# Kernel optimization log

Measured on AMD Instinct MI355X. Metric: run time of the kernel, lower is better.

Reference implementation:

```python
import jax, jax.numpy as jnp
import numpy as np

B, C, HF, WF = 2, 128, 60, 80
N = 3072
T = 16.0          # min(t_base + epoch, t_max), saturated
WIN_HALF = 0.125  # config['window_size'] (normalized half-width)
WIN_STEPS = 9     # window sampling grid side
EPS = 1e-6

def l2norm(x, axis):
    return x / jnp.sqrt(jnp.sum(x * x, axis=axis, keepdims=True) + 1e-12)

def denorm(cn, h, w):
    # normalized [-1,1] (x,y) -> pixel coords
    return (cn + 1.0) * 0.5 * jnp.array([w - 1.0, h - 1.0], cn.dtype)

def norm_coords(c, h, w):
    return c * (2.0 / jnp.array([w - 1.0, h - 1.0], c.dtype)) - 1.0

def bilinear_sample(fmap, cn):
    """fmap (b,C,H,W); cn (b,M,2) normalized (x,y); align_corners=True, border pad."""
    b, Cc, H, W = fmap.shape
    x = (cn[..., 0] + 1.0) * 0.5 * (W - 1)
    y = (cn[..., 1] + 1.0) * 0.5 * (H - 1)
    x0 = jnp.floor(x); y0 = jnp.floor(y)
    wx = x - x0; wy = y - y0
    x0i = jnp.clip(x0.astype(jnp.int32), 0, W - 1)
    x1i = jnp.clip(x0i + 1, 0, W - 1)
    y0i = jnp.clip(y0.astype(jnp.int32), 0, H - 1)
    y1i = jnp.clip(y0i + 1, 0, H - 1)
    gb = jax.vmap(lambda fm, yi, xi: fm[:, yi, xi])  # (C,M) per batch
    f00 = gb(fmap, y0i, x0i); f01 = gb(fmap, y0i, x1i)
    f10 = gb(fmap, y1i, x0i); f11 = gb(fmap, y1i, x1i)
    wx = wx[:, None, :]; wy = wy[:, None, :]
    out = f00 * (1 - wx) * (1 - wy) + f01 * wx * (1 - wy) + f10 * (1 - wx) * wy + f11 * wx * wy
    return jnp.transpose(out, (0, 2, 1))  # (b,M,C)

def window_search(feat1, fmap2_t, center_n):
    """Expected correspondence within a window. feat1 (b,N,C); fmap2_t pre-scaled by T."""
    b, n, Cc = feat1.shape
    lin = jnp.linspace(-WIN_HALF, WIN_HALF, WIN_STEPS).astype(feat1.dtype)
    gy, gx = jnp.meshgrid(lin, lin, indexing='ij')
    offs = jnp.stack([gx.ravel(), gy.ravel()], -1)         # (S,2)
    S = offs.shape[0]
    wc = center_n[:, :, None, :] + offs[None, None]         # (b,N,S,2)
    feats = bilinear_sample(fmap2_t, wc.reshape(b, n * S, 2)).reshape(b, n, S, Cc)
    prob = jax.nn.softmax(jnp.einsum('bnc,bnsc->bns', feat1, feats), axis=-1)
    exp_n = jnp.einsum('bns,bnsd->bnd', prob, wc)
    var = jnp.einsum('bns,bnsd->bnd', prob, wc ** 2) - exp_n ** 2
    std = jnp.sqrt(jnp.clip(var, EPS)).sum(-1)
    return exp_n, wc, std

def setup_inputs() -> dict:
    key = jax.random.key(0)
    k1, k2, k3, k4 = jax.random.split(key, 4)
    xf1 = jax.random.normal(k1, (B, C, HF, WF), jnp.float32)
    xf2 = jax.random.normal(k2, (B, C, HF, WF), jnp.float32)
    coord1_n = jax.random.uniform(k3, (B, N, 2), jnp.float32) * 2.0 - 1.0
    coord2_n = jax.random.uniform(k4, (B, N, 2), jnp.float32) * 2.0 - 1.0
    return {"xf1": xf1, "xf2": xf2, "coord1_n": coord1_n, "coord2_n": coord2_n,
            "h1i": 480, "w1i": 640, "h2i": 480, "w2i": 640}

def reference(xf1, xf2, coord1_n, coord2_n, h1i, w1i, h2i, w2i):
    coord1 = denorm(coord1_n, h1i, w1i)
    coord2 = denorm(coord2_n, h2i, w2i)
    f1 = l2norm(bilinear_sample(xf1, coord1_n), -1)  # cos distance -> L2-normalized
    f2 = l2norm(bilinear_sample(xf2, coord2_n), -1)
    cos_sim = jnp.einsum('bnc,bmc->bnm', f1, f2)      # (b,N,N)
    p12 = jax.nn.softmax(T * cos_sim, axis=2)
    p21 = jax.nn.softmax(T * cos_sim, axis=1)
    g1 = jnp.einsum('bnm,bmd->bnd', p12, coord2)      # feat1g_corloc
    g2 = jnp.einsum('bnm,bnd->bmd', p21, coord1)      # feat2g_corloc
    g1n = jax.lax.stop_gradient(norm_coords(g1, h2i, w2i))
    g2n = jax.lax.stop_gradient(norm_coords(g2, h1i, w1i))
    std1 = jnp.sqrt(jnp.clip(jnp.einsum('bnm,bmd->bnd', p12, coord2_n ** 2) - g1n ** 2, EPS)).sum(-1)
    std2 = jnp.sqrt(jnp.clip(jnp.einsum('bnm,bnd->bmd', p21, coord1_n ** 2) - g2n ** 2, EPS)).sum(-1)
    # use_line_search=False branch: window centers are the detached global corloc
    xf2t = T * l2norm(xf2, 1)
    xf1t = T * l2norm(xf1, 1)
    w1n, _, wstd1 = window_search(f1, xf2t, g1n)
    w2n, _, wstd2 = window_search(f2, xf1t, g2n)
    w1 = denorm(w1n, h2i, w2i)  # feat1w_corloc
    w2 = denorm(w2n, h1i, w1i)  # feat2w_corloc
    valid1 = jnp.ones(std1.shape, dtype=bool)
    valid2 = jnp.ones(std2.shape, dtype=bool)
    return (coord1, coord2, g1, g2, w1, w2, g1n, g2n, std1, std2, wstd1, wstd2, valid1, valid2)
```

## Files before the change

### kernel.cpp

```cpp
#include <hip/hip_runtime.h>
#include <hip/hip_bf16.h>
#include <math.h>

#define BB 2
#define CC 128
#define HH 60
#define WW 80
#define NN 3072
#define TT 16.0f
#define SS 81
#define HW (HH*WW)
#define NTILE 24
#define LDA 136
#define XN 12
#define YN 10
#define PSTRIDE 128

typedef __attribute__((ext_vector_type(8))) short short8;
typedef __attribute__((ext_vector_type(4))) float f32x4;
typedef _Float16 hf;
typedef _Float16 __attribute__((ext_vector_type(2))) h2;

#if __has_builtin(__builtin_amdgcn_fdot2)
#define FDOT2(a,b,c) __builtin_amdgcn_fdot2((a),(b),(c),false)
#else
#define FDOT2(a,b,c) ((c) + (float)(a).x*(float)(b).x + (float)(a).y*(float)(b).y)
#endif

template<int CTRL>
__device__ __forceinline__ float dppterm(float s){
    return __int_as_float(__builtin_amdgcn_update_dpp(0, __float_as_int(s), CTRL, 0xf, 0xf, true));
}
__device__ __forceinline__ float red8_add(float s){
    s += dppterm<0xB1>(s); s += dppterm<0x4E>(s); s += dppterm<0x141>(s); return s;
}
__device__ __forceinline__ float red16_add(float s){
    s += dppterm<0xB1>(s); s += dppterm<0x4E>(s); s += dppterm<0x141>(s); s += dppterm<0x140>(s); return s;
}
__device__ __forceinline__ float swz16_add(float s){
    return s + __int_as_float(__builtin_amdgcn_ds_swizzle(__float_as_int(s), 0x401F));
}
__device__ __forceinline__ float red64_add(float s){
    s = red16_add(s); s = swz16_add(s); s += __shfl_xor(s, 32); return s;
}
__device__ __forceinline__ float red64_max(float s){
    s = fmaxf(s, dppterm<0xB1>(s)); s = fmaxf(s, dppterm<0x4E>(s));
    s = fmaxf(s, dppterm<0x141>(s)); s = fmaxf(s, dppterm<0x140>(s));
    s = fmaxf(s, __int_as_float(__builtin_amdgcn_ds_swizzle(__float_as_int(s), 0x401F)));
    s = fmaxf(s, __shfl_xor(s, 32));
    return s;
}

__device__ __forceinline__ void bsetup(float cn, int L, int& i0, int& i1, float& w){
    float x = (cn + 1.0f) * 0.5f * (float)(L - 1);
    float x0 = floorf(x);
    w = x - x0;
    int xi = (int)x0;
    i0 = xi < 0 ? 0 : (xi > L - 1 ? L - 1 : xi);
    i1 = (i0 + 1 > L - 1) ? L - 1 : (i0 + 1);
}

__global__ __launch_bounds__(256) void k_normT(
        const float* __restrict__ xf1, const float* __restrict__ xf2,
        hf* __restrict__ xf1r, hf* __restrict__ xf2r,
        hf* __restrict__ xf1t, hf* __restrict__ xf2t){
    int idx = blockIdx.x;
    int map = idx / (BB*(HW/32));
    int rem = idx % (BB*(HW/32));
    int b   = rem / (HW/32);
    int hw0 = (rem % (HW/32)) * 32;
    const float* src = (map ? xf2 : xf1) + (size_t)b*CC*HW + hw0;
    hf* dstR = (map ? xf2r : xf1r) + ((size_t)(b*HW + hw0))*CC;
    hf* dstT = (map ? xf2t : xf1t) + ((size_t)(b*HW + hw0))*CC;

    __shared__ float tile[CC][33];
    int tid = threadIdx.x;
    {
        int p = tid & 31, c0 = tid >> 5;
        #pragma unroll
        for(int i=0;i<16;i++){
            int c = i*8 + c0;
            tile[c][p] = src[(size_t)c*HW + p];
        }
    }
    __syncthreads();
    int q = tid >> 3, l = tid & 7;
    float v[16];
    float ss = 0.f;
    #pragma unroll
    for(int k=0;k<16;k++){ v[k] = tile[l*16+k][q]; ss += v[k]*v[k]; }
    ss = red8_add(ss);
    float inv = 1.0f / sqrtf(ss + 1e-12f);
    float tsc = TT * inv;
    union { hf h[16]; uint4 u[2]; } R, T;
    #pragma unroll
    for(int k=0;k<16;k++){ R.h[k] = (hf)v[k]; T.h[k] = (hf)(v[k]*tsc); }
    uint4* oR = (uint4*)(dstR + (size_t)q*CC + l*16);
    uint4* oT = (uint4*)(dstT + (size_t)q*CC + l*16);
    oR[0] = R.u[0]; oR[1] = R.u[1];
    oT[0] = T.u[0]; oT[1] = T.u[1];
}

__global__ __launch_bounds__(256) void k_feats(
        const hf* __restrict__ xf1r, const hf* __restrict__ xf2r,
        const float* __restrict__ c1n, const float* __restrict__ c2n,
        __hip_bfloat16* __restrict__ f1b, __hip_bfloat16* __restrict__ f2b,
        float* __restrict__ o_coord1, float* __restrict__ o_coord2,
        const int* __restrict__ h1I, const int* __restrict__ w1I,
        const int* __restrict__ h2I, const int* __restrict__ w2I){
    int tid = threadIdx.x;
    int gid = blockIdx.x*4 + (tid >> 6);
    int dir = gid / (BB*NN);
    int bn  = gid % (BB*NN);
    int b = bn / NN;
    const hf* raw = dir ? xf2r : xf1r;
    const float* cn = dir ? c2n : c1n;
    __hip_bfloat16* fOutB = dir ? f2b : f1b;
    float* coordOut = dir ? o_coord2 : o_coord1;
    const int* hI = dir ? h2I : h1I;
    const int* wI = dir ? w2I : w1I;

    int t = tid & 63;
    float cnx = cn[(size_t)bn*2+0], cny = cn[(size_t)bn*2+1];
    int x0,x1,y0,y1; float wx,wy;
    bsetup(cnx, WW, x0,x1,wx);
    bsetup(cny, HH, y0,y1,wy);
    const hf* base = raw + (size_t)(b*HW)*CC;
    const uint* r00 = (const uint*)(base + (size_t)(y0*WW+x0)*CC) + t;
    const uint* r01 = (const uint*)(base + (size_t)(y0*WW+x1)*CC) + t;
    const uint* r10 = (const uint*)(base + (size_t)(y1*WW+x0)*CC) + t;
    const uint* r11 = (const uint*)(base + (size_t)(y1*WW+x1)*CC) + t;
    union { uint u; h2 v; } u00, u01, u10, u11;
    u00.u = *r00; u01.u = *r01; u10.u = *r10; u11.u = *r11;
    float w00=(1.f-wx)*(1.f-wy), w01=wx*(1.f-wy), w10=(1.f-wx)*wy, w11=wx*wy;
    float fx = w00*(float)u00.v.x + w01*(float)u01.v.x + w10*(float)u10.v.x + w11*(float)u11.v.x;
    float fy = w00*(float)u00.v.y + w01*(float)u01.v.y + w10*(float)u10.v.y + w11*(float)u11.v.y;
    float ss = fx*fx + fy*fy;
    ss = red64_add(ss);
    float inv = 1.0f / sqrtf(ss + 1e-12f);
    unsigned short blo = __bfloat16_as_ushort(__float2bfloat16(fx*inv));
    unsigned short bhi = __bfloat16_as_ushort(__float2bfloat16(fy*inv));
    ((uint*)(fOutB + (size_t)bn*CC))[t] = ((uint)bhi << 16) | blo;
    if(t==0){
        float h=(float)hI[0], w=(float)wI[0];
        coordOut[(size_t)bn*2+0] = (cnx+1.0f)*0.5f*(w-1.0f);
        coordOut[(size_t)bn*2+1] = (cny+1.0f)*0.5f*(h-1.0f);
    }
}

__global__ __launch_bounds__(512,4) void k_corr(
        const __hip_bfloat16* __restrict__ f1b, const __hip_bfloat16* __restrict__ f2b,
        const float* __restrict__ c1n, const float* __restrict__ c2n,
        float* __restrict__ wsP,
        const int* __restrict__ h1I, const int* __restrict__ w1I,
        const int* __restrict__ h2I, const int* __restrict__ w2I){
    const int nwg = BB*NTILE*NTILE;
    int blk = blockIdx.x;
    blk = (blk & 7)*(nwg/8) + (blk >> 3);
    int b   = blk / (NTILE*NTILE);
    int rem = blk % (NTILE*NTILE);
    int nt = rem / NTILE, mt = rem % NTILE;
    int n0 = nt*128, m0 = mt*128;
    int tid = threadIdx.x;
    int lane = tid & 63, wid = tid >> 6;
    int wr = wid >> 1, wc = wid & 1;
    int lr = lane & 15, lh = lane >> 4;

    __shared__ __align__(16) unsigned short smem[2*128*LDA];
    unsigned short* As = smem;
    unsigned short* Bs = smem + 128*LDA;
    float* parts = (float*)smem;
    const int COLOFF = 2*128*8;

    {
        const unsigned short* gA = (const unsigned short*)f1b + ((size_t)b*NN + n0)*CC;
        const unsigned short* gB = (const unsigned short*)f2b + ((size_t)b*NN + m0)*CC;
        #pragma unroll
        for(int it=0; it<4; ++it){
            int idx = tid + it*512;
            int r = idx >> 4, q = idx & 15;
            *(uint4*)(As + r*LDA + q*8) = *(const uint4*)(gA + r*CC + q*8);
            *(uint4*)(Bs + r*LDA + q*8) = *(const uint4*)(gB + r*CC + q*8);
        }
    }

    float2 c2v[4], c1v[8];
    #pragma unroll
    for(int j=0;j<4;j++)
        c2v[j] = ((const float2*)c2n)[(size_t)b*NN + m0 + wc*64 + j*16 + lr];
    #pragma unroll
    for(int i=0;i<2;i++)
        #pragma unroll
        for(int r=0;r<4;r++)
            c1v[i*4+r] = ((const float2*)c1n)[(size_t)b*NN + n0 + wr*32 + i*16 + lh*4 + r];

    __syncthreads();

    f32x4 acc[2][4] = {};
    const unsigned short* aBase = As + (wr*32 + lr)*LDA + lh*8;
    const unsigned short* bBase = Bs + (wc*64 + lr)*LDA + lh*8;
    #pragma unroll
    for(int ks=0; ks<4; ++ks){
        short8 afr[2], bfr[4];
        #pragma unroll
        for(int i=0;i<2;i++) afr[i] = *(const short8*)(aBase + i*16*LDA + ks*32);
        #pragma unroll
        for(int j=0;j<4;j++) bfr[j] = *(const short8*)(bBase + j*16*LDA + ks*32);
        #pragma unroll
        for(int i=0;i<2;i++)
            #pragma unroll
            for(int j=0;j<4;j++)
                acc[i][j] = __builtin_amdgcn_mfma_f32_16x16x32_bf16(afr[i], bfr[j], acc[i][j], 0,0,0);
    }
    __syncthreads();

    const float TL2E = 23.08312035f;
    float h1f=(float)h1I[0], w1f=(float)w1I[0], h2f=(float)h2I[0], w2f=(float)w2I[0];
    float sx2 = 0.5f*(w2f-1.0f), sy2 = 0.5f*(h2f-1.0f);
    float sx1 = 0.5f*(w1f-1.0f), sy1 = 0.5f*(h1f-1.0f);

    float cx2[4], cy2[4], cxx2[4], cyy2[4];
    #pragma unroll
    for(int j=0;j<4;j++){
        cx2[j] = (c2v[j].x+1.f)*sx2; cy2[j] = (c2v[j].y+1.f)*sy2;
        cxx2[j] = c2v[j].x*c2v[j].x; cyy2[j] = c2v[j].y*c2v[j].y;
    }
    float colA[4][5] = {};
    #pragma unroll
    for(int i=0;i<2;i++){
        #pragma unroll
        for(int r=0;r<4;r++){
            float2 c1 = c1v[i*4+r];
            float cx1=(c1.x+1.f)*sx1, cy1=(c1.y+1.f)*sy1;
            float cxx1=c1.x*c1.x, cyy1=c1.y*c1.y;
            float rs=0.f, rax=0.f, ray=0.f, raxx=0.f, rayy=0.f;
            #pragma unroll
            for(int j=0;j<4;j++){
                float wgt = exp2f(fmaf(TL2E, acc[i][j][r], -TL2E));
                rs += wgt;
                rax  = fmaf(wgt, cx2[j],  rax);
                ray  = fmaf(wgt, cy2[j],  ray);
                raxx = fmaf(wgt, cxx2[j], raxx);
                rayy = fmaf(wgt, cyy2[j], rayy);
                colA[j][0] += wgt;
                colA[j][1] = fmaf(wgt, cx1,  colA[j][1]);
                colA[j][2] = fmaf(wgt, cy1,  colA[j][2]);
                colA[j][3] = fmaf(wgt, cxx1, colA[j][3]);
                colA[j][4] = fmaf(wgt, cyy1, colA[j][4]);
            }
            rs   = red16_add(rs);
            rax  = red16_add(rax);
            ray  = red16_add(ray);
            raxx = red16_add(raxx);
            rayy = red16_add(rayy);
            if(lr==0){
                int nl = wr*32 + i*16 + lh*4 + r;
                float* rp = parts + ((size_t)wc*128 + nl)*8;
                *(float4*)rp = make_float4(rs, rax, ray, raxx);
                rp[4] = rayy;
            }
        }
    }
    #pragma unroll
    for(int j=0;j<4;j++){
        int ml = j*16 + lr;
        float* cp = parts + COLOFF + (((size_t)wid*4 + lh)*64 + ml)*6;
        *(float2*)cp     = make_float2(colA[j][0], colA[j][1]);
        *(float2*)(cp+2) = make_float2(colA[j][2], colA[j][3]);
        cp[4] = colA[j][4];
    }
    __syncthreads();

    if(tid < 128){
        int p = tid;
        float4 r0 = *(float4*)(parts + ((size_t)0*128 + p)*8);
        float  e0 = parts[((size_t)0*128 + p)*8 + 4];
        float4 r1 = *(float4*)(parts + ((size_t)1*128 + p)*8);
        float  e1 = parts[((size_t)1*128 + p)*8 + 4];
        float* o = wsP + ((size_t)b*NN + n0 + p)*PSTRIDE + mt*5;
        o[0] = r0.x + r1.x;
        o[1] = r0.y + r1.y;
        o[2] = r0.z + r1.z;
        o[3] = r0.w + r1.w;
        o[4] = e0 + e1;
    } else if(tid < 256){
        int p = tid - 128;
        int wcsel = p >> 6, pp = p & 63;
        float s0=0.f,s1=0.f,s2=0.f,s3=0.f,s4=0.f;
        #pragma unroll
        for(int wrv=0; wrv<4; ++wrv){
            #pragma unroll
            for(int lh2=0; lh2<4; ++lh2){
                const float* cp = parts + COLOFF + (((size_t)(wrv*2+wcsel)*4 + lh2)*64 + pp)*6;
                float2 a = *(const float2*)cp;
                float2 q = *(const float2*)(cp+2);
                s0 += a.x; s1 += a.y; s2 += q.x; s3 += q.y; s4 += cp[4];
            }
        }
        float* o = wsP + ((size_t)(BB*NN) + (size_t)b*NN + m0 + p)*PSTRIDE + nt*5;
        o[0]=s0; o[1]=s1; o[2]=s2; o[3]=s3; o[4]=s4;
    }
}

__global__ __launch_bounds__(256) void k_win2(
        const __hip_bfloat16* __restrict__ f1b, const __hip_bfloat16* __restrict__ f2b,
        const hf* __restrict__ xf1t, const hf* __restrict__ xf2t,
        const float* __restrict__ wsP,
        float* __restrict__ o_g1, float* __restrict__ o_g1n, float* __restrict__ o_std1,
        float* __restrict__ o_g2, float* __restrict__ o_g2n, float* __restrict__ o_std2,
        float* __restrict__ o_w1, float* __restrict__ o_wstd1,
        float* __restrict__ o_w2, float* __restrict__ o_wstd2,
        float* __restrict__ o_valid,
        const int* __restrict__ h1I, const int* __restrict__ w1I,
        const int* __restrict__ h2I, const int* __restrict__ w2I){
    int gid = blockIdx.x;
    int dir = gid / (BB*NN);
    int bn  = gid % (BB*NN);
    int b   = bn / NN;
    const __hip_bfloat16* fQ = dir ? f2b : f1b;
    const hf* fmapT          = dir ? xf1t : xf2t;
    const int* hI            = dir ? h1I  : h2I;
    const int* wI            = dir ? w1I  : w2I;
    float* outW              = dir ? o_w2 : o_w1;
    float* outStd            = dir ? o_wstd2 : o_wstd1;
    float* oG                = dir ? o_g2  : o_g1;
    float* oGn               = dir ? o_g2n : o_g1n;
    float* oSd               = dir ? o_std2: o_std1;

    int tid = threadIdx.x;
    int lane = tid & 63, wid = tid >> 6;
    int cg  = lane & 7;
    int sub = lane >> 3;

    __shared__ float acc5[5][25];
    {
        const float* base = wsP + ((size_t)dir*(BB*NN) + bn)*PSTRIDE;
        if(tid < NTILE*5){
            int mtc = tid/5, c = tid - mtc*5;
            acc5[c][mtc] = base[tid];
        }
    }
    __syncthreads();
    if(tid < 5){
        float s = 0.f;
        #pragma unroll
        for(int m=0;m<NTILE;m++) s += acc5[tid][m];
        acc5[tid][24] = s;
    }
    __syncthreads();
    float S = acc5[0][24], AX = acc5[1][24], AY = acc5[2][24];
    float AXX = acc5[3][24], AYY = acc5[4][24];
    float hfv = (float)hI[0], wfv = (float)wI[0];
    float gdx = AX/S, gdy = AY/S;
    float gx = gdx*(2.0f/(wfv-1.0f)) - 1.0f;
    float gy = gdy*(2.0f/(hfv-1.0f)) - 1.0f;
    if(tid == 0){
        float vx0 = AXX/S - gx*gx, vy0 = AYY/S - gy*gy;
        float sd0 = sqrtf(fmaxf(vx0,1e-6f)) + sqrtf(fmaxf(vy0,1e-6f));
        oG[(size_t)bn*2+0]=gdx; oG[(size_t)bn*2+1]=gdy;
        oGn[(size_t)bn*2+0]=gx; oGn[(size_t)bn*2+1]=gy;
        oSd[bn]=sd0;
        o_valid[gid]=1.0f;
    }

    int xb, yb;
    {   int t1; float tw;
        bsetup(gx - 0.125f, WW, xb, t1, tw);
        bsetup(gy - 0.125f, HH, yb, t1, tw);
    }

    h2 fq2[8];
    {
        const uint* q = (const uint*)(fQ + (size_t)bn*CC) + cg*8;
        #pragma unroll
        for(int d=0; d<8; ++d){
            uint u = q[d];
            float lo = __uint_as_float(u << 16);
            float hi = __uint_as_float(u & 0xffff0000u);
            fq2[d].x = (hf)lo; fq2[d].y = (hf)hi;
        }
    }

    __shared__ float dl[XN*YN];
    const hf* base = fmapT + (size_t)b*HW*CC;
    #pragma unroll
    for(int it=0; it<4; ++it){
        int p = wid*30 + it*8 + sub;
        bool act = (it < 3) || (sub < 6);
        int pc = act ? p : (wid*30 + 29);
        int ky = pc / XN, kx = pc - ky*XN;
        int py = yb + ky; if(py > HH-1) py = HH-1;
        int px = xb + kx; if(px > WW-1) px = WW-1;
        const uint4* row = (const uint4*)(base + (size_t)(py*WW + px)*CC) + cg*2;
        union { uint4 u[2]; h2 v[8]; } U;
        U.u[0] = row[0]; U.u[1] = row[1];
        float s = 0.f;
        #pragma unroll
        for(int d=0; d<8; ++d) s = FDOT2(fq2[d], U.v[d], s);
        s = red8_add(s);
        if(cg==0 && act) dl[p] = s;
    }
    __syncthreads();

    float logit = -INFINITY, wcx = 0.f, wcy = 0.f;
    if(tid < SS){
        int i = tid % 9, j = tid / 9;
        wcx = gx + (-0.125f + 0.03125f*(float)i);
        wcy = gy + (-0.125f + 0.03125f*(float)j);
        int x0,x1,y0,y1; float wx,wy;
        bsetup(wcx, WW, x0,x1,wx);
        bsetup(wcy, HH, y0,y1,wy);
        int r0 = (y0-yb)*XN - xb, r1 = (y1-yb)*XN - xb;
        float d00=dl[r0+x0], d01=dl[r0+x1], d10=dl[r1+x0], d11=dl[r1+x1];
        logit = d00*(1.f-wx)*(1.f-wy) + d01*wx*(1.f-wy) + d10*(1.f-wx)*wy + d11*wx*wy;
    }

    float M = red64_max(logit);
    __shared__ float mred[4];
    if(lane==0) mred[wid] = M;
    __syncthreads();
    M = fmaxf(fmaxf(mred[0],mred[1]), fmaxf(mred[2],mred[3]));

    float w = (tid < SS) ? __expf(logit - M) : 0.f;
    float v0 = red64_add(w);
    float v1 = red64_add(w*wcx);
    float v2 = red64_add(w*wcy);
    float v3 = red64_add(w*wcx*wcx);
    float v4 = red64_add(w*wcy*wcy);
    __shared__ float sred[4][5];
    if(lane==0){ sred[wid][0]=v0; sred[wid][1]=v1; sred[wid][2]=v2; sred[wid][3]=v3; sred[wid][4]=v4; }
    __syncthreads();
    if(tid==0){
        float Sw = sred[0][0]+sred[1][0]+sred[2][0]+sred[3][0];
        float ex = (sred[0][1]+sred[1][1]+sred[2][1]+sred[3][1])/Sw;
        float ey = (sred[0][2]+sred[1][2]+sred[2][2]+sred[3][2])/Sw;
        float vx = (sred[0][3]+sred[1][3]+sred[2][3]+sred[3][3])/Sw - ex*ex;
        float vy = (sred[0][4]+sred[1][4]+sred[2][4]+sred[3][4])/Sw - ey*ey;
        float sd = sqrtf(fmaxf(vx,1e-6f)) + sqrtf(fmaxf(vy,1e-6f));
        outW[(size_t)bn*2+0] = (ex+1.0f)*0.5f*(wfv-1.0f);
        outW[(size_t)bn*2+1] = (ey+1.0f)*0.5f*(hfv-1.0f);
        outStd[bn] = sd;
    }
}

extern "C" void kernel_launch(void* const* d_in, const int* in_sizes, int n_in,
                              void* d_out, int out_size, void* d_ws, size_t ws_size,
                              hipStream_t stream){
    const float* xf1 = (const float*)d_in[0];
    const float* xf2 = (const float*)d_in[1];
    const float* c1n = (const float*)d_in[2];
    const float* c2n = (const float*)d_in[3];
    const int* h1 = (const int*)d_in[4];
    const int* w1 = (const int*)d_in[5];
    const int* h2 = (const int*)d_in[6];
    const int* w2 = (const int*)d_in[7];
    float* out = (float*)d_out;

    hf* xf1r = (hf*)d_ws;
    hf* xf2r = xf1r + (size_t)BB*HW*CC;
    hf* xf1t = xf2r + (size_t)BB*HW*CC;
    hf* xf2t = xf1t + (size_t)BB*HW*CC;
    __hip_bfloat16* f1b = (__hip_bfloat16*)(xf2t + (size_t)BB*HW*CC);
    __hip_bfloat16* f2b = f1b + (size_t)BB*NN*CC;
    float* wsP = (float*)(f2b + (size_t)BB*NN*CC);

    float* o_coord1 = out + 0;
    float* o_coord2 = out + 12288;
    float* o_g1     = out + 24576;
    float* o_g2     = out + 36864;
    float* o_w1     = out + 49152;
    float* o_w2     = out + 61440;
    float* o_g1n    = out + 73728;
    float* o_g2n    = out + 86016;
    float* o_std1   = out + 98304;
    float* o_std2   = out + 104448;
    float* o_wstd1  = out + 110592;
    float* o_wstd2  = out + 116736;
    float* o_valid  = out + 122880;

    hipLaunchKernelGGL(k_normT, dim3(2*BB*(HW/32)), dim3(256), 0, stream,
                       xf1, xf2, xf1r, xf2r, xf1t, xf2t);
    hipLaunchKernelGGL(k_feats, dim3(2*BB*NN/4), dim3(256), 0, stream,
                       xf1r, xf2r, c1n, c2n, f1b, f2b, o_coord1, o_coord2, h1, w1, h2, w2);
    hipLaunchKernelGGL(k_corr, dim3(BB*NTILE*NTILE), dim3(512), 0, stream,
                       f1b, f2b, c1n, c2n, wsP, h1, w1, h2, w2);
    hipLaunchKernelGGL(k_win2, dim3(2*BB*NN), dim3(256), 0, stream,
                       f1b, f2b, xf1t, xf2t, wsP,
                       o_g1, o_g1n, o_std1, o_g2, o_g2n, o_std2,
                       o_w1, o_wstd1, o_w2, o_wstd2, o_valid, h1, w1, h2, w2);
}
```

Measured before the change: 69.72 us.

## Process one window-search query per wavefront instead of per block

The window-search kernel now gives each 64-lane wavefront its own query point, four per 256-thread block, instead of spreading one query across the whole block. Partial-sum reduction, the 120-cell dot-product grid, the softmax and the moment reductions all stay inside one wave, using shuffles and per-wave shared memory with no __syncthreads. This removes block-wide barriers and cross-wave shared-memory reductions and cuts the launched block count by four. In exchange each wave does 15 gather iterations serially and handles two window samples per lane, which lengthens the per-wave critical path.

```diff
diff --git a/kernel.cpp b/kernel.cpp
--- a/kernel.cpp
+++ b/kernel.cpp
@@ -313,7 +313,9 @@
         float* __restrict__ o_valid,
         const int* __restrict__ h1I, const int* __restrict__ w1I,
         const int* __restrict__ h2I, const int* __restrict__ w2I){
-    int gid = blockIdx.x;
+    int tid = threadIdx.x;
+    int lane = tid & 63, wid = tid >> 6;
+    int gid = blockIdx.x*4 + wid;
     int dir = gid / (BB*NN);
     int bn  = gid % (BB*NN);
     int b   = bn / NN;
@@ -327,34 +329,27 @@
     float* oGn               = dir ? o_g2n : o_g1n;
     float* oSd               = dir ? o_std2: o_std1;
 
-    int tid = threadIdx.x;
-    int lane = tid & 63, wid = tid >> 6;
-    int cg  = lane & 7;
-    int sub = lane >> 3;
-
-    __shared__ float acc5[5][25];
-    {
-        const float* base = wsP + ((size_t)dir*(BB*NN) + bn)*PSTRIDE;
-        if(tid < NTILE*5){
-            int mtc = tid/5, c = tid - mtc*5;
-            acc5[c][mtc] = base[tid];
-        }
-    }
-    __syncthreads();
-    if(tid < 5){
-        float s = 0.f;
-        #pragma unroll
-        for(int m=0;m<NTILE;m++) s += acc5[tid][m];
-        acc5[tid][24] = s;
-    }
-    __syncthreads();
-    float S = acc5[0][24], AX = acc5[1][24], AY = acc5[2][24];
-    float AXX = acc5[3][24], AYY = acc5[4][24];
+    __shared__ float dlS[4][128];
+    float* dl = dlS[wid];
+
+    const float* basep = wsP + ((size_t)dir*(BB*NN) + bn)*PSTRIDE;
+    dl[lane] = basep[lane];
+    if(lane < 56) dl[64+lane] = basep[64+lane];
+    float partc = 0.f;
+    if(lane < 5){
+        #pragma unroll
+        for(int m=0;m<NTILE;m++) partc += dl[m*5+lane];
+    }
+    float S  = __shfl(partc, 0);
+    float AX = __shfl(partc, 1);
+    float AY = __shfl(partc, 2);
+    float AXX= __shfl(partc, 3);
+    float AYY= __shfl(partc, 4);
     float hfv = (float)hI[0], wfv = (float)wI[0];
     float gdx = AX/S, gdy = AY/S;
     float gx = gdx*(2.0f/(wfv-1.0f)) - 1.0f;
     float gy = gdy*(2.0f/(hfv-1.0f)) - 1.0f;
-    if(tid == 0){
+    if(lane == 0){
         float vx0 = AXX/S - gx*gx, vy0 = AYY/S - gy*gy;
         float sd0 = sqrtf(fmaxf(vx0,1e-6f)) + sqrtf(fmaxf(vy0,1e-6f));
         oG[(size_t)bn*2+0]=gdx; oG[(size_t)bn*2+1]=gdy;
@@ -368,6 +363,8 @@
         bsetup(gx - 0.125f, WW, xb, t1, tw);
         bsetup(gy - 0.125f, HH, yb, t1, tw);
     }
+    int cg  = lane & 7;
+    int sub = lane >> 3;
 
     h2 fq2[8];
     {
@@ -381,14 +378,11 @@
         }
     }
 
-    __shared__ float dl[XN*YN];
     const hf* base = fmapT + (size_t)b*HW*CC;
-    #pragma unroll
-    for(int it=0; it<4; ++it){
-        int p = wid*30 + it*8 + sub;
-        bool act = (it < 3) || (sub < 6);
-        int pc = act ? p : (wid*30 + 29);
-        int ky = pc / XN, kx = pc - ky*XN;
+    #pragma unroll 5
+    for(int it=0; it<15; ++it){
+        int p = it*8 + sub;
+        int ky = p / XN, kx = p - ky*XN;
         int py = yb + ky; if(py > HH-1) py = HH-1;
         int px = xb + kx; if(px > WW-1) px = WW-1;
         const uint4* row = (const uint4*)(base + (size_t)(py*WW + px)*CC) + cg*2;
@@ -398,44 +392,47 @@
         #pragma unroll
         for(int d=0; d<8; ++d) s = FDOT2(fq2[d], U.v[d], s);
         s = red8_add(s);
-        if(cg==0 && act) dl[p] = s;
-    }
-    __syncthreads();
-
-    float logit = -INFINITY, wcx = 0.f, wcy = 0.f;
-    if(tid < SS){
-        int i = tid % 9, j = tid / 9;
-        wcx = gx + (-0.125f + 0.03125f*(float)i);
-        wcy = gy + (-0.125f + 0.03125f*(float)j);
+        if(cg==0) dl[p] = s;
+    }
+
+    float l0, wx0c, wy0c;
+    {
+        int i = lane % 9, j = lane / 9;
+        wx0c = gx + (-0.125f + 0.03125f*(float)i);
+        wy0c = gy + (-0.125f + 0.03125f*(float)j);
         int x0,x1,y0,y1; float wx,wy;
-        bsetup(wcx, WW, x0,x1,wx);
-        bsetup(wcy, HH, y0,y1,wy);
+        bsetup(wx0c, WW, x0,x1,wx);
+        bsetup(wy0c, HH, y0,y1,wy);
         int r0 = (y0-yb)*XN - xb, r1 = (y1-yb)*XN - xb;
         float d00=dl[r0+x0], d01=dl[r0+x1], d10=dl[r1+x0], d11=dl[r1+x1];
-        logit = d00*(1.f-wx)*(1.f-wy) + d01*wx*(1.f-wy) + d10*(1.f-wx)*wy + d11*wx*wy;
-    }
-
-    float M = red64_max(logit);
-    __shared__ float mred[4];
-    if(lane==0) mred[wid] = M;
-    __syncthreads();
-    M = fmaxf(fmaxf(mred[0],mred[1]), fmaxf(mred[2],mred[3]));
-
-    float w = (tid < SS) ? __expf(logit - M) : 0.f;
-    float v0 = red64_add(w);
-    float v1 = red64_add(w*wcx);
-    float v2 = red64_add(w*wcy);
-    float v3 = red64_add(w*wcx*wcx);
-    float v4 = red64_add(w*wcy*wcy);
-    __shared__ float sred[4][5];
-    if(lane==0){ sred[wid][0]=v0; sred[wid][1]=v1; sred[wid][2]=v2; sred[wid][3]=v3; sred[wid][4]=v4; }
-    __syncthreads();
-    if(tid==0){
-        float Sw = sred[0][0]+sred[1][0]+sred[2][0]+sred[3][0];
-        float ex = (sred[0][1]+sred[1][1]+sred[2][1]+sred[3][1])/Sw;
-        float ey = (sred[0][2]+sred[1][2]+sred[2][2]+sred[3][2])/Sw;
-        float vx = (sred[0][3]+sred[1][3]+sred[2][3]+sred[3][3])/Sw - ex*ex;
-        float vy = (sred[0][4]+sred[1][4]+sred[2][4]+sred[3][4])/Sw - ey*ey;
+        l0 = d00*(1.f-wx)*(1.f-wy) + d01*wx*(1.f-wy) + d10*(1.f-wx)*wy + d11*wx*wy;
+    }
+    float l1 = -INFINITY, wx1c = 0.f, wy1c = 0.f;
+    if(lane < SS-64){
+        int s1 = 64 + lane;
+        int i = s1 % 9, j = s1 / 9;
+        wx1c = gx + (-0.125f + 0.03125f*(float)i);
+        wy1c = gy + (-0.125f + 0.03125f*(float)j);
+        int x0,x1,y0,y1; float wx,wy;
+        bsetup(wx1c, WW, x0,x1,wx);
+        bsetup(wy1c, HH, y0,y1,wy);
+        int r0 = (y0-yb)*XN - xb, r1 = (y1-yb)*XN - xb;
+        float d00=dl[r0+x0], d01=dl[r0+x1], d10=dl[r1+x0], d11=dl[r1+x1];
+        l1 = d00*(1.f-wx)*(1.f-wy) + d01*wx*(1.f-wy) + d10*(1.f-wx)*wy + d11*wx*wy;
+    }
+
+    float M = red64_max(fmaxf(l0, l1));
+    float w0 = __expf(l0 - M);
+    float w1 = (lane < SS-64) ? __expf(l1 - M) : 0.f;
+    float v0 = red64_add(w0 + w1);
+    float v1 = red64_add(w0*wx0c + w1*wx1c);
+    float v2 = red64_add(w0*wy0c + w1*wy1c);
+    float v3 = red64_add(w0*wx0c*wx0c + w1*wx1c*wx1c);
+    float v4 = red64_add(w0*wy0c*wy0c + w1*wy1c*wy1c);
+    if(lane == 0){
+        float ex = v1/v0, ey = v2/v0;
+        float vx = v3/v0 - ex*ex;
+        float vy = v4/v0 - ey*ey;
         float sd = sqrtf(fmaxf(vx,1e-6f)) + sqrtf(fmaxf(vy,1e-6f));
         outW[(size_t)bn*2+0] = (ex+1.0f)*0.5f*(wfv-1.0f);
         outW[(size_t)bn*2+1] = (ey+1.0f)*0.5f*(hfv-1.0f);
@@ -484,7 +481,7 @@
                        xf1r, xf2r, c1n, c2n, f1b, f2b, o_coord1, o_coord2, h1, w1, h2, w2);
     hipLaunchKernelGGL(k_corr, dim3(BB*NTILE*NTILE), dim3(512), 0, stream,
                        f1b, f2b, c1n, c2n, wsP, h1, w1, h2, w2);
-    hipLaunchKernelGGL(k_win2, dim3(2*BB*NN), dim3(256), 0, stream,
+    hipLaunchKernelGGL(k_win2, dim3(2*BB*NN/4), dim3(256), 0, stream,
                        f1b, f2b, xf1t, xf2t, wsP,
                        o_g1, o_g1n, o_std1, o_g2, o_g2n, o_std2,
                        o_w1, o_wstd1, o_w2, o_wstd2, o_valid, h1, w1, h2, w2);
```

After: 61.73 us (median of 2 runs). 1.13x faster.
